# Kernel optimization log

Measured on AMD Instinct MI355X. Metric: run time of the kernel, lower is better.

Reference implementation:

```python
import jax, jax.numpy as jnp
import numpy as np

M_HIST = 6
LAM = 1e-4
THRESHOLD = 50
BETA = 1.0


def _f_step(z, x, Wh, bh, Wx, bx, Wo, bo):
    # DEQ cell: f(z, x) = tanh(Linear(tanh(h_layer(x) + x_layer(z))))
    # (note: Func.forward(x, z) is called as f(z, x), so h_layer sees the
    #  external input x and x_layer sees the iterate z)
    hidden = jnp.tanh(x @ Wh.T + bh + z @ Wx.T + bx)  # [B,S,H]
    return jnp.tanh(hidden @ Wo.T + bo)               # [B,S,D]


def _anderson(f, x0):
    bsz = x0.shape[0]
    dL = x0.shape[1] * x0.shape[2]
    flat = lambda z: z.reshape(bsz, dL)
    unflat = lambda z: z.reshape(x0.shape)

    X = jnp.zeros((bsz, M_HIST, dL), dtype=x0.dtype)
    F = jnp.zeros((bsz, M_HIST, dL), dtype=x0.dtype)
    F0 = flat(f(x0))
    X = X.at[:, 0].set(flat(x0))
    F = F.at[:, 0].set(F0)
    X = X.at[:, 1].set(F0)
    F = F.at[:, 1].set(flat(f(unflat(F0))))

    lowest = jnp.asarray(1e8, dtype=x0.dtype)
    lowest_x = jnp.zeros((bsz, dL), dtype=x0.dtype)

    for k in range(2, THRESHOLD):  # fixed unrolled solver iterations
        n = min(k, M_HIST)
        G = F[:, :n] - X[:, :n]                       # [B,n,dL]
        GG = jnp.einsum('bnd,bmd->bnm', G, G) + LAM * jnp.eye(n, dtype=x0.dtype)
        H = jnp.zeros((bsz, n + 1, n + 1), dtype=x0.dtype)
        H = H.at[:, 0, 1:].set(1.0)
        H = H.at[:, 1:, 0].set(1.0)
        H = H.at[:, 1:, 1:].set(GG)
        rhs = jnp.zeros((bsz, n + 1, 1), dtype=x0.dtype).at[:, 0, 0].set(1.0)
        alpha = jnp.linalg.solve(H, rhs)[:, 1:, 0]    # [B,n]
        Xk = BETA * jnp.einsum('bn,bnd->bd', alpha, F[:, :n]) \
            + (1.0 - BETA) * jnp.einsum('bn,bnd->bd', alpha, X[:, :n])
        Fk = flat(f(unflat(Xk)))
        X = X.at[:, k % M_HIST].set(Xk)
        F = F.at[:, k % M_HIST].set(Fk)
        abs_diff = jnp.linalg.norm(Fk - Xk)
        rel_diff = abs_diff / (1e-5 + jnp.linalg.norm(Fk))
        better = rel_diff < lowest
        lowest_x = jnp.where(better, Xk, lowest_x)
        lowest = jnp.minimum(rel_diff, lowest)
    return unflat(lowest_x)


def setup_inputs() -> dict:
    key = jax.random.key(0)
    ks = jax.random.split(key, 9)
    B, S, D, H, O = 16384, 31, 14, 50, 1
    sc = lambda fan_in: 1.0 / np.sqrt(fan_in)
    return {
        'x':  jax.random.normal(ks[0], (B, S, D), jnp.float32),
        'Wh': jax.random.normal(ks[1], (H, D), jnp.float32) * sc(D),
        'bh': jax.random.normal(ks[2], (H,), jnp.float32) * sc(D),
        'Wx': jax.random.normal(ks[3], (H, D), jnp.float32) * sc(D),
        'bx': jax.random.normal(ks[4], (H,), jnp.float32) * sc(D),
        'Wo': jax.random.normal(ks[5], (D, H), jnp.float32) * sc(H),
        'bo': jax.random.normal(ks[6], (D,), jnp.float32) * sc(H),
        'Wf': jax.random.normal(ks[7], (O, S * D), jnp.float32) * sc(S * D),
        'bf': jax.random.normal(ks[8], (O,), jnp.float32) * sc(S * D),
    }


def reference(x, Wh, bh, Wx, bx, Wo, bo, Wf, bf):
    f = lambda z: _f_step(z, x, Wh, bh, Wx, bx, Wo, bo)
    z_star = _anderson(f, jnp.zeros_like(x))   # fixed-point solve (no grad)
    z = f(z_star)                              # one extra f application
    out = z.reshape(z.shape[0], -1) @ Wf.T + bf  # [B,1]
    return out
```

## Files before the change

### kernel.cpp

```cpp
#include <hip/hip_runtime.h>
#include <hip/hip_fp16.h>

#define S 31
#define D 14
#define H 50
#define NB 16384
#define NITER 48
#define LAMR 1e-4f
#define TSC 2.8853900817779268f

#define WS_D2   0
#define WS_F2   64
#define WS_WHP  128
#define WS_BHX  928
#define WS_BO   992
#define WS_WX2  1024
#define WS_WO2  1424
#define WS_WF2  1792
#define WS_OUTK 4096

typedef _Float16 f16x2 __attribute__((ext_vector_type(2)));

#if defined(__has_builtin) && __has_builtin(__builtin_amdgcn_rcpf)
#define FRCP(x) __builtin_amdgcn_rcpf(x)
#else
#define FRCP(x) (1.0f/(x))
#endif

#if defined(__has_builtin) && __has_builtin(__builtin_amdgcn_exp2f)
#define FEXP2(x) __builtin_amdgcn_exp2f(x)
#else
#define FEXP2(x) exp2f(x)
#endif

#define FDOT2(a,b,c) __builtin_amdgcn_fdot2((a),(b),(c),false)

__device__ __forceinline__ f16x2 pkrtz(float a, float b){
  auto r = __builtin_amdgcn_cvt_pkrtz(a, b);
  return __builtin_bit_cast(f16x2, r);
}
#define PKRTZ(a,b) pkrtz((a),(b))

__device__ __forceinline__ f16x2 pack_rn(float a, float b){
  __half2 h = __floats2half2_rn(a, b);
  return __builtin_bit_cast(f16x2, h);
}

template<int CTRL>
__device__ __forceinline__ float dppadd(float v){
  int pv = __builtin_amdgcn_update_dpp(0, __builtin_bit_cast(int, v),
                                       CTRL, 0xF, 0xF, true);
  return v + __builtin_bit_cast(float, pv);
}

#define AIJ(i,j) ((i)*6 - ((i)*((i)+1))/2 + (j))

__device__ __forceinline__ float tfast(float x){
  float e = FEXP2(x);
  return 1.f - 2.f * FRCP(e + 1.f);
}

__global__ void prep_kernel(const float* __restrict__ Wh, const float* __restrict__ bh,
                            const float* __restrict__ Wx, const float* __restrict__ bx,
                            const float* __restrict__ Wo, const float* __restrict__ bo,
                            const float* __restrict__ Wf, float* __restrict__ ws){
  int t = threadIdx.x;
  for (int i=t;i<128;i+=256) ws[i]=0.f;
  for (int i=t;i<800;i+=256){
    int h=i>>4, d=i&15;
    ws[WS_WHP+i] = (d<D)? Wh[h*D+d]*TSC : 0.f;
  }
  for (int i=t;i<64;i+=256) ws[WS_BHX+i] = (i<H)? (bh[i]+bx[i])*TSC : 0.f;
  for (int i=t;i<16;i+=256) ws[WS_BO+i]  = (i<D)? bo[i]*TSC : 0.f;
  __half2* wx2 = (__half2*)(ws + WS_WX2);
  for (int i=t;i<400;i+=256){
    int h=i>>3, dd=i&7, d0=2*dd, d1=2*dd+1;
    float a=(d0<D)?Wx[h*D+d0]*TSC:0.f, b=(d1<D)?Wx[h*D+d1]*TSC:0.f;
    wx2[i] = __floats2half2_rn(a,b);
  }
  __half2* wo2 = (__half2*)(ws + WS_WO2);
  for (int i=t;i<364;i+=256){
    int d=i/26, hh=i-26*d, h0=2*hh, h1=2*hh+1;
    float a=(hh<25)?Wo[d*H+h0]*TSC:0.f, b=(hh<25)?Wo[d*H+h1]*TSC:0.f;
    wo2[i] = __floats2half2_rn(a,b);
  }
  __half2* wf2 = (__half2*)(ws + WS_WF2);
  for (int i=t;i<256;i+=256){
    int s=i>>3, dd=i&7, d0=2*dd, d1=2*dd+1;
    float a=(s<S && d0<D)?Wf[s*D+d0]:0.f, b=(s<S && d1<D)?Wf[s*D+d1]:0.f;
    wf2[i] = __floats2half2_rn(a,b);
  }
}

#define FEVAL() do{ \
  float oacc_[14]; \
  _Pragma("unroll") for (int d_=0; d_<14; ++d_) oacc_[d_] = bop[d_]; \
  _Pragma("unroll") \
  for (int hh_=0; hh_<25; ++hh_){ \
    f16x2 hx2_ = hxr2[hh_]; \
    float a0_ = (float)hx2_[0], b0_ = (float)hx2_[1]; \
    _Pragma("unroll") for (int q_=0;q_<7;++q_){ \
      a0_ = FDOT2(xvh[q_], wx2[(2*hh_)*8+q_],   a0_); \
      b0_ = FDOT2(xvh[q_], wx2[(2*hh_+1)*8+q_], b0_); } \
    f16x2 th_ = PKRTZ(tfast(a0_), tfast(b0_)); \
    _Pragma("unroll") for (int d_=0; d_<14; ++d_) \
      oacc_[d_] = FDOT2(th_, wo2[d_*26+hh_], oacc_[d_]); \
  } \
  _Pragma("unroll") for (int dp_=0; dp_<7; ++dp_) \
    fvh[dp_] = PKRTZ(tfast(oacc_[2*dp_]), tfast(oacc_[2*dp_+1])); \
}while(0)

#define ZERO_INACT() do{ \
  if (!act){ \
    _Pragma("unroll") for (int q_=0;q_<7;++q_){ fvh[q_]=zzv; gvh[q_]=zzv; } \
  } \
}while(0)

#define PUSHB(DOPROJ) do{ \
  float rv_[8]; \
  _Pragma("unroll") for (int j_=0;j_<5;++j_){ \
    float acc_=0.f; \
    _Pragma("unroll") for (int q_=0;q_<7;++q_) acc_ = FDOT2(gvh[q_], Gh[(j_+1)*7+q_], acc_); \
    rv_[j_] = acc_; } \
  d2l=0.f; f2l=0.f; \
  _Pragma("unroll") for (int q_=0;q_<7;++q_){ \
    d2l = FDOT2(gvh[q_], gvh[q_], d2l); \
    f2l = FDOT2(fvh[q_], fvh[q_], f2l); } \
  rv_[5]=d2l; rv_[6]=f2l; rv_[7]=0.f; \
  if (DOPROJ){ \
    float pa_=0.f; \
    _Pragma("unroll") for (int q_=0;q_<7;++q_) pa_ = FDOT2(fvh[q_], wfr[q_], pa_); \
    rv_[7]=pa_; } \
  _Pragma("unroll") for (int i_=0;i_<8;++i_) rv_[i_] = dppadd<0x121>(rv_[i_]); \
  _Pragma("unroll") for (int i_=0;i_<8;++i_) rv_[i_] = dppadd<0x122>(rv_[i_]); \
  _Pragma("unroll") for (int i_=0;i_<8;++i_) rv_[i_] = dppadd<0x124>(rv_[i_]); \
  _Pragma("unroll") for (int i_=0;i_<8;++i_) rv_[i_] = dppadd<0x128>(rv_[i_]); \
  _Pragma("unroll") for (int i_=0;i_<8;++i_) rv_[i_] += __shfl_xor(rv_[i_], 16); \
  d2r = rv_[5]; f2r = rv_[6]; po_red = rv_[7]; \
  _Pragma("unroll") for (int j_=0;j_<5;++j_) \
    _Pragma("unroll") for (int q_=0;q_<7;++q_){ \
      Fh[j_*7+q_] = Fh[(j_+1)*7+q_]; Gh[j_*7+q_] = Gh[(j_+1)*7+q_]; } \
  _Pragma("unroll") for (int q_=0;q_<7;++q_){ Fh[35+q_]=fvh[q_]; Gh[35+q_]=gvh[q_]; } \
  _Pragma("unroll") for (int i_=0;i_<5;++i_) \
    _Pragma("unroll") for (int j_=i_;j_<5;++j_) GG[AIJ(i_,j_)] = GG[AIJ(i_+1,j_+1)]; \
  _Pragma("unroll") for (int j_=0;j_<5;++j_) GG[AIJ(j_,5)] = rv_[j_]; \
  GG[AIJ(5,5)] = d2r; \
}while(0)

__global__ __launch_bounds__(64, 3)
void solver_kernel(const float* __restrict__ x,
                   const float* __restrict__ whp, const float* __restrict__ bhx,
                   const float* __restrict__ bop,
                   const f16x2* __restrict__ wx2, const f16x2* __restrict__ wo2,
                   const f16x2* __restrict__ wf2,
                   float* __restrict__ outk, float* __restrict__ d2p, float* __restrict__ f2p){
  const int tid  = threadIdx.x;
  const int lane = tid & 63;
  const int s    = tid & 31;
  const int elem = blockIdx.x*2 + (tid>>5);
  const bool act = (s < S);

  __shared__ f16x2 hx2_sh[64*27];
  f16x2* hxw2 = hx2_sh + tid*27;

  {
    float xd[D];
#pragma unroll
    for (int d=0; d<D; ++d) xd[d]=0.f;
    if (act){
      const float* xr = x + ((size_t)elem*S + s)*D;
#pragma unroll
      for (int d=0; d<D; ++d) xd[d]=xr[d];
    }
#pragma unroll 5
    for (int hp=0; hp<25; ++hp){
      float a0 = bhx[2*hp], a1 = bhx[2*hp+1];
#pragma unroll
      for (int d=0; d<D; ++d){
        a0 += xd[d]*whp[(2*hp)*16+d];
        a1 += xd[d]*whp[(2*hp+1)*16+d];
      }
      hxw2[hp] = pack_rn(a0, a1);
    }
  }
  const f16x2* hxr2 = hxw2;
  const f16x2 zzv = {(_Float16)0.f, (_Float16)0.f};
  const f16x2* wfr = wf2 + s*8;

  f16x2 Fh[42], Gh[42], xvh[7], fvh[7], gvh[7];
  float GG[21];
  float d2l, f2l, d2r, f2r, po_red;
#pragma unroll
  for (int i=0;i<42;++i){ Fh[i]=zzv; Gh[i]=zzv; }
#pragma unroll
  for (int i=0;i<21;++i) GG[i]=0.f;

#pragma unroll
  for (int q=0;q<7;++q) xvh[q]=zzv;
  FEVAL();
#pragma unroll
  for (int q=0;q<7;++q) gvh[q]=fvh[q]-xvh[q];
  ZERO_INACT();
  PUSHB(0);
#pragma unroll
  for (int q=0;q<7;++q) xvh[q]=fvh[q];
  FEVAL();
#pragma unroll
  for (int q=0;q<7;++q) gvh[q]=fvh[q]-xvh[q];
  ZERO_INACT();
  PUSHB(0);

#pragma unroll 1
  for (int kk=2; kk<50; ++kk){
    float A_[21], invd[6], yv[6];
    if (kk >= 6){
#pragma unroll
      for (int i=0;i<6;++i)
#pragma unroll
        for (int j=i;j<6;++j) A_[AIJ(i,j)] = GG[AIJ(i,j)] + ((i==j)?LAMR:0.f);
    } else {
      int lo = 6-kk;
#pragma unroll
      for (int i=0;i<6;++i)
#pragma unroll
        for (int j=i;j<6;++j){
          float v = GG[AIJ(i,j)] + ((i==j)?LAMR:0.f);
          A_[AIJ(i,j)] = (i>=lo)? v : ((i==j)?1e30f:0.f);
        }
    }
#pragma unroll
    for (int i=0;i<6;++i) yv[i]=1.f;
#pragma unroll
    for (int p=0;p<6;++p){
      invd[p] = FRCP(A_[AIJ(p,p)]);
#pragma unroll
      for (int i=p+1;i<6;++i){
        float m = A_[AIJ(p,i)]*invd[p];
#pragma unroll
        for (int j=i;j<6;++j) A_[AIJ(i,j)] -= m*A_[AIJ(p,j)];
        yv[i] -= m*yv[p];
      }
    }
#pragma unroll
    for (int p=5;p>=0;--p){
      float acc=yv[p];
#pragma unroll
      for (int j=p+1;j<6;++j) acc -= A_[AIJ(p,j)]*yv[j];
      yv[p]=acc*invd[p];
    }
    float isum = FRCP(yv[0]+yv[1]+yv[2]+yv[3]+yv[4]+yv[5]);
#pragma unroll
    for (int q=0;q<7;++q) xvh[q]=zzv;
#pragma unroll
    for (int j=0;j<6;++j){
      _Float16 ah = (_Float16)(yv[j]*isum);
      f16x2 a2 = {ah, ah};
#pragma unroll
      for (int q=0;q<7;++q) xvh[q] += a2*Fh[j*7+q];
    }
    FEVAL();
#pragma unroll
    for (int q=0;q<7;++q) gvh[q]=fvh[q]-xvh[q];
    ZERO_INACT();
    PUSHB(1);
    float d2w = d2r + __shfl_xor(d2r, 32);
    float f2w = f2r + __shfl_xor(f2r, 32);
    if (lane==0){ atomicAdd(&d2p[kk-2], d2w); atomicAdd(&f2p[kk-2], f2w); }
    if (s==0) outk[(size_t)(kk-2)*NB + elem] = po_red;
  }
}

__global__ void final_kernel(const float* __restrict__ d2p, const float* __restrict__ f2p,
                             const float* __restrict__ outk, const float* __restrict__ bf,
                             float* __restrict__ out){
  int b = blockIdx.x*blockDim.x + threadIdx.x;
  float best = 1e8f; int kst = 0;
  for (int k=0;k<NITER;++k){
    float rel = sqrtf(d2p[k]) / (1e-5f + sqrtf(f2p[k]));
    if (rel < best){ best = rel; kst = k; }
  }
  out[b] = outk[(size_t)kst*NB + b] + bf[0];
}

extern "C" void kernel_launch(void* const* d_in, const int* in_sizes, int n_in,
                              void* d_out, int out_size, void* d_ws, size_t ws_size,
                              hipStream_t stream){
  const float* x  = (const float*)d_in[0];
  const float* Wh = (const float*)d_in[1];
  const float* bh = (const float*)d_in[2];
  const float* Wx = (const float*)d_in[3];
  const float* bx = (const float*)d_in[4];
  const float* Wo = (const float*)d_in[5];
  const float* bo = (const float*)d_in[6];
  const float* Wf = (const float*)d_in[7];
  const float* bf = (const float*)d_in[8];
  float* ws  = (float*)d_ws;
  float* out = (float*)d_out;

  hipLaunchKernelGGL(prep_kernel, dim3(1), dim3(256), 0, stream, Wh,bh,Wx,bx,Wo,bo,Wf,ws);
  hipLaunchKernelGGL(solver_kernel, dim3(NB/2), dim3(64), 0, stream,
                     x, ws+WS_WHP, ws+WS_BHX, ws+WS_BO,
                     (const f16x2*)(ws+WS_WX2), (const f16x2*)(ws+WS_WO2), (const f16x2*)(ws+WS_WF2),
                     ws+WS_OUTK, ws+WS_D2, ws+WS_F2);
  hipLaunchKernelGGL(final_kernel, dim3(NB/256), dim3(256), 0, stream,
                     ws+WS_D2, ws+WS_F2, ws+WS_OUTK, bf, out);
}
```

Before: 2.808 ms.

## Move DEQ cell evaluation onto MFMA 16x16x32 fp16 matrix ops

Replaces the per-thread scalar fdot2 evaluation of the two dense layers with MFMA 16x16x32 fp16 instructions over a 64-row tile (two batch elements × 32 positions). Wh, Wx and the fused biases are concatenated into a single K=32 weight matrix, with a constant 1 column carrying the bias; the iterate and input are staged in LDS, and the hidden activations go through a swizzled LDS buffer. The Anderson history is redistributed to the MFMA output layout and the bootstrap iterations are folded into the main loop. This cuts VALU dot-product work but adds LDS traffic and layout shuffles, and keeps fp16 precision risk.

```diff
diff --git a/kernel.cpp b/kernel.cpp
--- a/kernel.cpp
+++ b/kernel.cpp
@@ -11,15 +11,14 @@
 
 #define WS_D2   0
 #define WS_F2   64
-#define WS_WHP  128
-#define WS_BHX  928
-#define WS_BO   992
-#define WS_WX2  1024
-#define WS_WO2  1424
-#define WS_WF2  1792
+#define WS_WC1  128
+#define WS_WOC  1152
+#define WS_WF   1664
 #define WS_OUTK 4096
 
 typedef _Float16 f16x2 __attribute__((ext_vector_type(2)));
+typedef _Float16 f16x8 __attribute__((ext_vector_type(8)));
+typedef float    f32x4 __attribute__((ext_vector_type(4)));
 
 #if defined(__has_builtin) && __has_builtin(__builtin_amdgcn_rcpf)
 #define FRCP(x) __builtin_amdgcn_rcpf(x)
@@ -38,12 +37,6 @@
 __device__ __forceinline__ f16x2 pkrtz(float a, float b){
   auto r = __builtin_amdgcn_cvt_pkrtz(a, b);
   return __builtin_bit_cast(f16x2, r);
-}
-#define PKRTZ(a,b) pkrtz((a),(b))
-
-__device__ __forceinline__ f16x2 pack_rn(float a, float b){
-  __half2 h = __floats2half2_rn(a, b);
-  return __builtin_bit_cast(f16x2, h);
 }
 
 template<int CTRL>
@@ -66,207 +59,250 @@
                             const float* __restrict__ Wf, float* __restrict__ ws){
   int t = threadIdx.x;
   for (int i=t;i<128;i+=256) ws[i]=0.f;
-  for (int i=t;i<800;i+=256){
-    int h=i>>4, d=i&15;
-    ws[WS_WHP+i] = (d<D)? Wh[h*D+d]*TSC : 0.f;
-  }
-  for (int i=t;i<64;i+=256) ws[WS_BHX+i] = (i<H)? (bh[i]+bx[i])*TSC : 0.f;
-  for (int i=t;i<16;i+=256) ws[WS_BO+i]  = (i<D)? bo[i]*TSC : 0.f;
-  __half2* wx2 = (__half2*)(ws + WS_WX2);
-  for (int i=t;i<400;i+=256){
-    int h=i>>3, dd=i&7, d0=2*dd, d1=2*dd+1;
-    float a=(d0<D)?Wx[h*D+d0]*TSC:0.f, b=(d1<D)?Wx[h*D+d1]*TSC:0.f;
-    wx2[i] = __floats2half2_rn(a,b);
-  }
-  __half2* wo2 = (__half2*)(ws + WS_WO2);
-  for (int i=t;i<364;i+=256){
-    int d=i/26, hh=i-26*d, h0=2*hh, h1=2*hh+1;
-    float a=(hh<25)?Wo[d*H+h0]*TSC:0.f, b=(hh<25)?Wo[d*H+h1]*TSC:0.f;
-    wo2[i] = __floats2half2_rn(a,b);
-  }
-  __half2* wf2 = (__half2*)(ws + WS_WF2);
+  __half2* wc1 = (__half2*)(ws + WS_WC1);
+  for (int i=t;i<1024;i+=256){
+    int n=i>>4, kp=i&15, k0=2*kp, k1=2*kp+1;
+    float v0=0.f, v1=0.f;
+    if (n<H){
+      v0 = (k0<14)? Wh[n*D+k0]*TSC : (k0<28)? Wx[n*D+(k0-14)]*TSC : (k0==28)? (bh[n]+bx[n])*TSC : 0.f;
+      v1 = (k1<14)? Wh[n*D+k1]*TSC : (k1<28)? Wx[n*D+(k1-14)]*TSC : (k1==28)? (bh[n]+bx[n])*TSC : 0.f;
+    }
+    wc1[i] = __floats2half2_rn(v0,v1);
+  }
+  __half2* woc = (__half2*)(ws + WS_WOC);
+  for (int i=t;i<512;i+=256){
+    int d=i>>5, kp=i&31, k0=2*kp, k1=2*kp+1;
+    float v0=0.f, v1=0.f;
+    if (d<D){
+      v0 = (k0<H)? Wo[d*H+k0]*TSC : (k0==H)? bo[d]*TSC : 0.f;
+      v1 = (k1<H)? Wo[d*H+k1]*TSC : (k1==H)? bo[d]*TSC : 0.f;
+    }
+    woc[i] = __floats2half2_rn(v0,v1);
+  }
+  __half2* wf = (__half2*)(ws + WS_WF);
   for (int i=t;i<256;i+=256){
-    int s=i>>3, dd=i&7, d0=2*dd, d1=2*dd+1;
-    float a=(s<S && d0<D)?Wf[s*D+d0]:0.f, b=(s<S && d1<D)?Wf[s*D+d1]:0.f;
-    wf2[i] = __floats2half2_rn(a,b);
-  }
-}
-
-#define FEVAL() do{ \
-  float oacc_[14]; \
-  _Pragma("unroll") for (int d_=0; d_<14; ++d_) oacc_[d_] = bop[d_]; \
-  _Pragma("unroll") \
-  for (int hh_=0; hh_<25; ++hh_){ \
-    f16x2 hx2_ = hxr2[hh_]; \
-    float a0_ = (float)hx2_[0], b0_ = (float)hx2_[1]; \
-    _Pragma("unroll") for (int q_=0;q_<7;++q_){ \
-      a0_ = FDOT2(xvh[q_], wx2[(2*hh_)*8+q_],   a0_); \
-      b0_ = FDOT2(xvh[q_], wx2[(2*hh_+1)*8+q_], b0_); } \
-    f16x2 th_ = PKRTZ(tfast(a0_), tfast(b0_)); \
-    _Pragma("unroll") for (int d_=0; d_<14; ++d_) \
-      oacc_[d_] = FDOT2(th_, wo2[d_*26+hh_], oacc_[d_]); \
-  } \
-  _Pragma("unroll") for (int dp_=0; dp_<7; ++dp_) \
-    fvh[dp_] = PKRTZ(tfast(oacc_[2*dp_]), tfast(oacc_[2*dp_+1])); \
-}while(0)
-
-#define ZERO_INACT() do{ \
-  if (!act){ \
-    _Pragma("unroll") for (int q_=0;q_<7;++q_){ fvh[q_]=zzv; gvh[q_]=zzv; } \
-  } \
-}while(0)
-
-#define PUSHB(DOPROJ) do{ \
-  float rv_[8]; \
-  _Pragma("unroll") for (int j_=0;j_<5;++j_){ \
-    float acc_=0.f; \
-    _Pragma("unroll") for (int q_=0;q_<7;++q_) acc_ = FDOT2(gvh[q_], Gh[(j_+1)*7+q_], acc_); \
-    rv_[j_] = acc_; } \
-  d2l=0.f; f2l=0.f; \
-  _Pragma("unroll") for (int q_=0;q_<7;++q_){ \
-    d2l = FDOT2(gvh[q_], gvh[q_], d2l); \
-    f2l = FDOT2(fvh[q_], fvh[q_], f2l); } \
-  rv_[5]=d2l; rv_[6]=f2l; rv_[7]=0.f; \
-  if (DOPROJ){ \
-    float pa_=0.f; \
-    _Pragma("unroll") for (int q_=0;q_<7;++q_) pa_ = FDOT2(fvh[q_], wfr[q_], pa_); \
-    rv_[7]=pa_; } \
-  _Pragma("unroll") for (int i_=0;i_<8;++i_) rv_[i_] = dppadd<0x121>(rv_[i_]); \
-  _Pragma("unroll") for (int i_=0;i_<8;++i_) rv_[i_] = dppadd<0x122>(rv_[i_]); \
-  _Pragma("unroll") for (int i_=0;i_<8;++i_) rv_[i_] = dppadd<0x124>(rv_[i_]); \
-  _Pragma("unroll") for (int i_=0;i_<8;++i_) rv_[i_] = dppadd<0x128>(rv_[i_]); \
-  _Pragma("unroll") for (int i_=0;i_<8;++i_) rv_[i_] += __shfl_xor(rv_[i_], 16); \
-  d2r = rv_[5]; f2r = rv_[6]; po_red = rv_[7]; \
-  _Pragma("unroll") for (int j_=0;j_<5;++j_) \
-    _Pragma("unroll") for (int q_=0;q_<7;++q_){ \
-      Fh[j_*7+q_] = Fh[(j_+1)*7+q_]; Gh[j_*7+q_] = Gh[(j_+1)*7+q_]; } \
-  _Pragma("unroll") for (int q_=0;q_<7;++q_){ Fh[35+q_]=fvh[q_]; Gh[35+q_]=gvh[q_]; } \
-  _Pragma("unroll") for (int i_=0;i_<5;++i_) \
-    _Pragma("unroll") for (int j_=i_;j_<5;++j_) GG[AIJ(i_,j_)] = GG[AIJ(i_+1,j_+1)]; \
-  _Pragma("unroll") for (int j_=0;j_<5;++j_) GG[AIJ(j_,5)] = rv_[j_]; \
-  GG[AIJ(5,5)] = d2r; \
-}while(0)
+    int s=i>>3, dp=i&7, d0=2*dp, d1=2*dp+1;
+    float v0=(s<S&&d0<D)?Wf[s*D+d0]:0.f, v1=(s<S&&d1<D)?Wf[s*D+d1]:0.f;
+    wf[i] = __floats2half2_rn(v0,v1);
+  }
+}
 
 __global__ __launch_bounds__(64, 3)
 void solver_kernel(const float* __restrict__ x,
-                   const float* __restrict__ whp, const float* __restrict__ bhx,
-                   const float* __restrict__ bop,
-                   const f16x2* __restrict__ wx2, const f16x2* __restrict__ wo2,
-                   const f16x2* __restrict__ wf2,
+                   const f16x8* __restrict__ wc1, const f16x8* __restrict__ woc,
+                   const f16x2* __restrict__ wf,
                    float* __restrict__ outk, float* __restrict__ d2p, float* __restrict__ f2p){
-  const int tid  = threadIdx.x;
-  const int lane = tid & 63;
-  const int s    = tid & 31;
-  const int elem = blockIdx.x*2 + (tid>>5);
-  const bool act = (s < S);
-
-  __shared__ f16x2 hx2_sh[64*27];
-  f16x2* hxw2 = hx2_sh + tid*27;
-
+  const int l = threadIdx.x;
+  const int a = l & 15;
+  const int g = l >> 4;
+  const int elemA = blockIdx.x*2;
+
+  __shared__ __align__(16) unsigned char AZ[4096];
+  __shared__ __align__(16) unsigned char HB[8192];
+
+#pragma unroll
+  for (int i=0;i<16;++i) *(float*)(AZ + l*64 + i*4) = 0.f;
   {
-    float xd[D];
-#pragma unroll
-    for (int d=0; d<D; ++d) xd[d]=0.f;
-    if (act){
-      const float* xr = x + ((size_t)elem*S + s)*D;
-#pragma unroll
-      for (int d=0; d<D; ++d) xd[d]=xr[d];
-    }
-#pragma unroll 5
-    for (int hp=0; hp<25; ++hp){
-      float a0 = bhx[2*hp], a1 = bhx[2*hp+1];
-#pragma unroll
-      for (int d=0; d<D; ++d){
-        a0 += xd[d]*whp[(2*hp)*16+d];
-        a1 += xd[d]*whp[(2*hp+1)*16+d];
-      }
-      hxw2[hp] = pack_rn(a0, a1);
-    }
-  }
-  const f16x2* hxr2 = hxw2;
-  const f16x2 zzv = {(_Float16)0.f, (_Float16)0.f};
-  const f16x2* wfr = wf2 + s*8;
-
-  f16x2 Fh[42], Gh[42], xvh[7], fvh[7], gvh[7];
+    int s = l & 31, e = l >> 5;
+    if (s < S){
+      const float* xr = x + ((size_t)(elemA+e)*S + s)*D;
+#pragma unroll
+      for (int i=0;i<7;++i){
+        __half2 h2 = __floats2half2_rn(xr[2*i], xr[2*i+1]);
+        *(f16x2*)(AZ + l*64 + i*4) = __builtin_bit_cast(f16x2, h2);
+      }
+    }
+    *(_Float16*)(AZ + l*64 + 56) = (_Float16)1.0f;
+  }
+  const f16x2 wfr0 = wf[a*8+g*2],      wfr1 = wf[a*8+g*2+1];
+  const f16x2 wfr2 = wf[(16+a)*8+g*2], wfr3 = wf[(16+a)*8+g*2+1];
+
+  const f16x2 zz = {(_Float16)0.f,(_Float16)0.f};
+  const int zo0 = 28 + g*8;
+  const int zo1 = (g==3) ? 60 : 32 + g*8;
+
+  f16x2 Fh[48], Gh[48], fo[8];
   float GG[21];
-  float d2l, f2l, d2r, f2r, po_red;
-#pragma unroll
-  for (int i=0;i<42;++i){ Fh[i]=zzv; Gh[i]=zzv; }
+#pragma unroll
+  for (int i=0;i<48;++i){ Fh[i]=zz; Gh[i]=zz; }
 #pragma unroll
   for (int i=0;i<21;++i) GG[i]=0.f;
 
-#pragma unroll
-  for (int q=0;q<7;++q) xvh[q]=zzv;
-  FEVAL();
-#pragma unroll
-  for (int q=0;q<7;++q) gvh[q]=fvh[q]-xvh[q];
-  ZERO_INACT();
-  PUSHB(0);
-#pragma unroll
-  for (int q=0;q<7;++q) xvh[q]=fvh[q];
-  FEVAL();
-#pragma unroll
-  for (int q=0;q<7;++q) gvh[q]=fvh[q]-xvh[q];
-  ZERO_INACT();
-  PUSHB(0);
-
 #pragma unroll 1
-  for (int kk=2; kk<50; ++kk){
-    float A_[21], invd[6], yv[6];
-    if (kk >= 6){
-#pragma unroll
-      for (int i=0;i<6;++i)
-#pragma unroll
-        for (int j=i;j<6;++j) A_[AIJ(i,j)] = GG[AIJ(i,j)] + ((i==j)?LAMR:0.f);
-    } else {
-      int lo = 6-kk;
-#pragma unroll
-      for (int i=0;i<6;++i)
-#pragma unroll
-        for (int j=i;j<6;++j){
-          float v = GG[AIJ(i,j)] + ((i==j)?LAMR:0.f);
-          A_[AIJ(i,j)] = (i>=lo)? v : ((i==j)?1e30f:0.f);
+  for (int kk=0; kk<50; ++kk){
+    if (kk >= 2){
+      float A_[21], yv[6];
+      if (kk >= 6){
+#pragma unroll
+        for (int i=0;i<6;++i)
+#pragma unroll
+          for (int j=i;j<6;++j) A_[AIJ(i,j)] = GG[AIJ(i,j)] + ((i==j)?LAMR:0.f);
+      } else {
+        int lo = 6-kk;
+#pragma unroll
+        for (int i=0;i<6;++i)
+#pragma unroll
+          for (int j=i;j<6;++j){
+            float v = GG[AIJ(i,j)] + ((i==j)?LAMR:0.f);
+            A_[AIJ(i,j)] = (i>=lo)? v : ((i==j)?1e30f:0.f);
+          }
+      }
+#pragma unroll
+      for (int i=0;i<6;++i) yv[i]=1.f;
+#pragma unroll
+      for (int p=0;p<6;++p){
+        float ip = FRCP(A_[AIJ(p,p)]);
+        A_[AIJ(p,p)] = ip;
+#pragma unroll
+        for (int i=p+1;i<6;++i){
+          float m = A_[AIJ(p,i)]*ip;
+#pragma unroll
+          for (int j=i;j<6;++j) A_[AIJ(i,j)] -= m*A_[AIJ(p,j)];
+          yv[i] -= m*yv[p];
         }
-    }
-#pragma unroll
-    for (int i=0;i<6;++i) yv[i]=1.f;
-#pragma unroll
-    for (int p=0;p<6;++p){
-      invd[p] = FRCP(A_[AIJ(p,p)]);
-#pragma unroll
-      for (int i=p+1;i<6;++i){
-        float m = A_[AIJ(p,i)]*invd[p];
-#pragma unroll
-        for (int j=i;j<6;++j) A_[AIJ(i,j)] -= m*A_[AIJ(p,j)];
-        yv[i] -= m*yv[p];
-      }
-    }
-#pragma unroll
-    for (int p=5;p>=0;--p){
-      float acc=yv[p];
-#pragma unroll
-      for (int j=p+1;j<6;++j) acc -= A_[AIJ(p,j)]*yv[j];
-      yv[p]=acc*invd[p];
-    }
-    float isum = FRCP(yv[0]+yv[1]+yv[2]+yv[3]+yv[4]+yv[5]);
-#pragma unroll
-    for (int q=0;q<7;++q) xvh[q]=zzv;
-#pragma unroll
-    for (int j=0;j<6;++j){
-      _Float16 ah = (_Float16)(yv[j]*isum);
-      f16x2 a2 = {ah, ah};
-#pragma unroll
-      for (int q=0;q<7;++q) xvh[q] += a2*Fh[j*7+q];
-    }
-    FEVAL();
-#pragma unroll
-    for (int q=0;q<7;++q) gvh[q]=fvh[q]-xvh[q];
-    ZERO_INACT();
-    PUSHB(1);
-    float d2w = d2r + __shfl_xor(d2r, 32);
-    float f2w = f2r + __shfl_xor(f2r, 32);
-    if (lane==0){ atomicAdd(&d2p[kk-2], d2w); atomicAdd(&f2p[kk-2], f2w); }
-    if (s==0) outk[(size_t)(kk-2)*NB + elem] = po_red;
+      }
+#pragma unroll
+      for (int p=5;p>=0;--p){
+        float acc=yv[p];
+#pragma unroll
+        for (int j=p+1;j<6;++j) acc -= A_[AIJ(p,j)]*yv[j];
+        yv[p]=acc*A_[AIJ(p,p)];
+      }
+      float isum = FRCP(yv[0]+yv[1]+yv[2]+yv[3]+yv[4]+yv[5]);
+      f16x2 xk[8];
+#pragma unroll
+      for (int i=0;i<8;++i) xk[i]=zz;
+#pragma unroll
+      for (int j=0;j<6;++j){
+        float ao = yv[j]*isum;
+        float ot = __shfl_xor(ao, 32);
+        float vA = (l<32)? ao : ot;
+        float vB = (l<32)? ot : ao;
+        _Float16 hA=(_Float16)vA, hB=(_Float16)vB;
+        f16x2 a2A={hA,hA}, a2B={hB,hB};
+#pragma unroll
+        for (int i=0;i<4;++i) xk[i] += a2A*Fh[j*8+i];
+#pragma unroll
+        for (int i=4;i<8;++i) xk[i] += a2B*Fh[j*8+i];
+      }
+#pragma unroll
+      for (int nt=0;nt<4;++nt){
+        int r = nt*16 + a;
+        *(f16x2*)(AZ + r*64 + zo0) = xk[nt*2];
+        *(f16x2*)(AZ + r*64 + zo1) = xk[nt*2+1];
+      }
+    } else if (kk == 1){
+#pragma unroll
+      for (int nt=0;nt<4;++nt){
+        int r = nt*16 + a;
+        *(f16x2*)(AZ + r*64 + zo0) = fo[nt*2];
+        *(f16x2*)(AZ + r*64 + zo1) = fo[nt*2+1];
+      }
+    }
+#pragma unroll
+    for (int nt=0;nt<4;++nt){
+      f16x8 B = wc1[(nt*16+a)*4 + g];
+#pragma unroll
+      for (int mt=0;mt<4;++mt){
+        f16x8 A = *(const f16x8*)(AZ + (mt*16+a)*64 + g*16);
+        f32x4 c = {0.f,0.f,0.f,0.f};
+        c = __builtin_amdgcn_mfma_f32_16x16x32_f16(A, B, c, 0,0,0);
+#pragma unroll
+        for (int q=0;q<4;++q){
+          int r = mt*16 + g*4 + q;
+          _Float16 hv = (_Float16)tfast(c[q]);
+          if (nt==3 && a==2) hv = (_Float16)1.0f;
+          *(_Float16*)(HB + ((r*128 + (nt*16+a)*2) ^ ((r&7)<<4))) = hv;
+        }
+      }
+    }
+    {
+      f16x8 wA0 = woc[a*8 + g], wA1 = woc[a*8 + 4 + g];
+#pragma unroll
+      for (int nt=0;nt<4;++nt){
+        int r2 = nt*16 + a;
+        f16x8 b0 = *(const f16x8*)(HB + ((r2*128 +  0 + g*16) ^ ((r2&7)<<4)));
+        f16x8 b1 = *(const f16x8*)(HB + ((r2*128 + 64 + g*16) ^ ((r2&7)<<4)));
+        f32x4 c = {0.f,0.f,0.f,0.f};
+        c = __builtin_amdgcn_mfma_f32_16x16x32_f16(wA0, b0, c, 0,0,0);
+        c = __builtin_amdgcn_mfma_f32_16x16x32_f16(wA1, b1, c, 0,0,0);
+        fo[nt*2]   = pkrtz(tfast(c[0]), tfast(c[1]));
+        fo[nt*2+1] = pkrtz(tfast(c[2]), tfast(c[3]));
+      }
+    }
+    f16x2 go[8];
+#pragma unroll
+    for (int nt=0;nt<4;++nt){
+      int r = nt*16 + a;
+      f16x2 x0 = *(const f16x2*)(AZ + r*64 + zo0);
+      f16x2 x1 = *(const f16x2*)(AZ + r*64 + zo1);
+      go[nt*2]   = fo[nt*2]   - x0;
+      go[nt*2+1] = fo[nt*2+1] - x1;
+    }
+    if (a == 15){
+      fo[2]=zz; fo[3]=zz; fo[6]=zz; fo[7]=zz;
+      go[2]=zz; go[3]=zz; go[6]=zz; go[7]=zz;
+    }
+#pragma unroll
+    for (int j=0;j<5;++j)
+#pragma unroll
+      for (int i=0;i<8;++i){ Fh[j*8+i]=Fh[(j+1)*8+i]; Gh[j*8+i]=Gh[(j+1)*8+i]; }
+#pragma unroll
+    for (int i=0;i<8;++i){ Fh[40+i]=fo[i]; Gh[40+i]=go[i]; }
+    float rv[16];
+#pragma unroll
+    for (int j=0;j<5;++j){
+      float pa=0.f, pb=0.f;
+#pragma unroll
+      for (int i=0;i<4;++i) pa = FDOT2(Gh[40+i], Gh[j*8+i], pa);
+#pragma unroll
+      for (int i=4;i<8;++i) pb = FDOT2(Gh[40+i], Gh[j*8+i], pb);
+      rv[j]=pa; rv[8+j]=pb;
+    }
+    {
+      float pa=0.f,pb=0.f,qa=0.f,qb=0.f,ra=0.f,rb=0.f;
+#pragma unroll
+      for (int i=0;i<4;++i){
+        pa = FDOT2(Gh[40+i], Gh[40+i], pa);
+        qa = FDOT2(Fh[40+i], Fh[40+i], qa);
+      }
+#pragma unroll
+      for (int i=4;i<8;++i){
+        pb = FDOT2(Gh[40+i], Gh[40+i], pb);
+        qb = FDOT2(Fh[40+i], Fh[40+i], qb);
+      }
+      ra = FDOT2(Fh[40+0], wfr0, ra); ra = FDOT2(Fh[40+1], wfr1, ra);
+      ra = FDOT2(Fh[40+2], wfr2, ra); ra = FDOT2(Fh[40+3], wfr3, ra);
+      rb = FDOT2(Fh[44+0], wfr0, rb); rb = FDOT2(Fh[44+1], wfr1, rb);
+      rb = FDOT2(Fh[44+2], wfr2, rb); rb = FDOT2(Fh[44+3], wfr3, rb);
+      rv[5]=pa; rv[13]=pb; rv[6]=qa; rv[14]=qb; rv[7]=ra; rv[15]=rb;
+    }
+#pragma unroll
+    for (int i=0;i<16;++i) rv[i] = dppadd<0x121>(rv[i]);
+#pragma unroll
+    for (int i=0;i<16;++i) rv[i] = dppadd<0x122>(rv[i]);
+#pragma unroll
+    for (int i=0;i<16;++i) rv[i] = dppadd<0x124>(rv[i]);
+#pragma unroll
+    for (int i=0;i<16;++i) rv[i] = dppadd<0x128>(rv[i]);
+#pragma unroll
+    for (int i=0;i<16;++i) rv[i] += __shfl_xor(rv[i],16);
+#pragma unroll
+    for (int i=0;i<16;++i) rv[i] += __shfl_xor(rv[i],32);
+    const bool eB = (l >= 32);
+#pragma unroll
+    for (int i_=0;i_<5;++i_)
+#pragma unroll
+      for (int j_=i_;j_<5;++j_) GG[AIJ(i_,j_)] = GG[AIJ(i_+1,j_+1)];
+#pragma unroll
+    for (int j=0;j<5;++j) GG[AIJ(j,5)] = eB? rv[8+j] : rv[j];
+    GG[AIJ(5,5)] = eB? rv[13] : rv[5];
+    if (kk>=2 && l==0){
+      atomicAdd(&d2p[kk-2], rv[5]+rv[13]);
+      atomicAdd(&f2p[kk-2], rv[6]+rv[14]);
+      outk[(size_t)(kk-2)*NB + elemA]     = rv[7];
+      outk[(size_t)(kk-2)*NB + elemA + 1] = rv[15];
+    }
   }
 }
 
@@ -299,8 +335,8 @@
 
   hipLaunchKernelGGL(prep_kernel, dim3(1), dim3(256), 0, stream, Wh,bh,Wx,bx,Wo,bo,Wf,ws);
   hipLaunchKernelGGL(solver_kernel, dim3(NB/2), dim3(64), 0, stream,
-                     x, ws+WS_WHP, ws+WS_BHX, ws+WS_BO,
-                     (const f16x2*)(ws+WS_WX2), (const f16x2*)(ws+WS_WO2), (const f16x2*)(ws+WS_WF2),
+                     x, (const f16x8*)(ws+WS_WC1), (const f16x8*)(ws+WS_WOC),
+                     (const f16x2*)(ws+WS_WF),
                      ws+WS_OUTK, ws+WS_D2, ws+WS_F2);
   hipLaunchKernelGGL(final_kernel, dim3(NB/256), dim3(256), 0, stream,
                      ws+WS_D2, ws+WS_F2, ws+WS_OUTK, bf, out);
```

Measured after the change: 4.166 ms. +48.4%, slower.
